# Kernel optimization log

Measured on AMD Instinct MI355X. Metric: run time of the kernel, lower is better.

The kernel has to match this reference:

```python
import jax, jax.numpy as jnp
import numpy as np

N_NODES = 100000
N_EDGES = 3200000
D_NODE = 5            # per-node feature dim
D_IN = 2 * D_NODE     # 10, MLP input dim
D_HID = D_IN * 5      # 50, HIDDEN_DIM_MULTIPLIER = 5


def setup_inputs() -> dict:
    key = jax.random.key(0)
    ks = jax.random.split(key, 8)
    x = jax.random.normal(ks[0], (N_NODES, D_NODE), dtype=jnp.float32)
    edge_index = jax.random.randint(ks[1], (2, N_EDGES), 0, N_NODES, dtype=jnp.int64)
    s1 = 1.0 / np.sqrt(D_IN)
    s2 = 1.0 / np.sqrt(D_HID)
    W1 = jax.random.uniform(ks[2], (D_IN, D_HID), jnp.float32, -s1, s1)
    b1 = jax.random.uniform(ks[3], (D_HID,), jnp.float32, -s1, s1)
    W2 = jax.random.uniform(ks[4], (D_HID, D_HID), jnp.float32, -s2, s2)
    b2 = jax.random.uniform(ks[5], (D_HID,), jnp.float32, -s2, s2)
    W3 = jax.random.uniform(ks[6], (D_HID, 1), jnp.float32, -s2, s2)
    b3 = jax.random.uniform(ks[7], (1,), jnp.float32, -s2, s2)
    return {"x": x, "edge_index": edge_index, "W1": W1, "b1": b1,
            "W2": W2, "b2": b2, "W3": W3, "b3": b3}


def reference(x, edge_index, W1, b1, W2, b2, W3, b3):
    # gather src/tgt node features and concat -> [E, 2*D_NODE]
    ef = jnp.concatenate([x[edge_index[0]], x[edge_index[1]]], axis=-1)
    h = jax.nn.relu(ef @ W1 + b1)
    h = jax.nn.relu(h @ W2 + b2)
    return jax.nn.sigmoid(h @ W3 + b3)  # [E, 1]
```

## Files before the change

kernel.cpp:

```cpp
#include <hip/hip_runtime.h>
#include <hip/hip_bf16.h>

typedef short bf16x8 __attribute__((ext_vector_type(8)));
typedef float f32x4  __attribute__((ext_vector_type(4)));

__device__ inline ushort f2bf(float f) {
    union { float f; uint u; } v; v.f = f;
    uint r = (v.u + 0x7FFFu + ((v.u >> 16) & 1u)) >> 16;
    return (ushort)r;
}
__device__ inline uint packbf(float a, float b) {
    float2 t; t.x = a; t.y = b;
    __hip_bfloat162 h = __float22bfloat162_rn(t);
    union { __hip_bfloat162 h; uint u; } cv; cv.h = h; return cv.u;
}

__global__ __launch_bounds__(256) void pack_x_kernel(
    const float* __restrict__ x, uint4* __restrict__ xp, int N)
{
    int i = blockIdx.x * blockDim.x + threadIdx.x;
    if (i > N) return;
    uint4 o = {0u, 0u, 0u, 0u};
    if (i < N) {
        const float* r = x + (size_t)i * 5;
        o.x = packbf(r[0], r[1]);
        o.y = packbf(r[2], r[3]);
        o.z = packbf(r[4], 1.0f);
    }
    xp[i] = o;
}

__global__ __launch_bounds__(64) void pack_w_kernel(
    const float* __restrict__ W1, const float* __restrict__ b1,
    const float* __restrict__ W2, const float* __restrict__ b2,
    const float* __restrict__ W3, uint4* __restrict__ tab)
{
    const int lane = threadIdx.x;
    const int c = lane & 15;
    const int g = lane >> 4;

    union { ushort s[8]; uint4 q; } u;
    #pragma unroll
    for (int mt = 0; mt < 4; ++mt) {
        #pragma unroll
        for (int d = 0; d < 8; ++d) {
            int k = 8 * g + d;
            int j = 16 * mt + c;
            float v = 0.f;
            if (j < 50) {
                if (k < 5)                 v = W1[k * 50 + j];
                else if (k == 5)           v = b1[j];
                else if (k >= 8 && k < 13) v = W1[(k - 3) * 50 + j];
            } else if (j == 50 && k == 5)  v = 1.0f;
            u.s[d] = f2bf(v);
        }
        tab[mt * 64 + lane] = u.q;
    }
    #pragma unroll
    for (int t = 0; t < 2; ++t) {
        #pragma unroll
        for (int mt = 0; mt < 4; ++mt) {
            #pragma unroll
            for (int d = 0; d < 8; ++d) {
                int hid1 = 16 * (2 * t + (d >> 2)) + 4 * g + (d & 3);
                int j    = 16 * mt + c;
                float v = 0.f;
                if (j < 50) {
                    if (hid1 < 50)       v = W2[hid1 * 50 + j];
                    else if (hid1 == 50) v = b2[j];
                }
                u.s[d] = f2bf(v);
            }
            tab[(4 + t * 4 + mt) * 64 + lane] = u.q;
        }
    }
    union { float f[4]; uint4 q; } wq;
    #pragma unroll
    for (int mt = 0; mt < 4; ++mt) {
        #pragma unroll
        for (int r = 0; r < 4; ++r) {
            int h = 16 * mt + 4 * g + r;
            wq.f[r] = (h < 50) ? W3[h] : 0.f;
        }
        tab[(12 + mt) * 64 + lane] = wq.q;
    }
}

__global__ __launch_bounds__(256, 4) void edge_mlp_mfma4(
    const uint4* __restrict__ xp,
    const uint4* __restrict__ wtab,
    const int* __restrict__ ei,
    const float* __restrict__ b3,
    float* __restrict__ out, int E, int N, int num_tiles)
{
    __shared__ uint4 lds_frag[1024];

    const int tid = threadIdx.x;
    #pragma unroll
    for (int i = 0; i < 4; ++i) lds_frag[tid + 256 * i] = wtab[tid + 256 * i];
    __syncthreads();

    const int w    = tid >> 6;
    const int lane = tid & 63;
    const int c    = lane & 15;
    const int g    = lane >> 4;

    bf16x8 w1f[4];
    #pragma unroll
    for (int mt = 0; mt < 4; ++mt)
        w1f[mt] = *(const bf16x8*)&lds_frag[mt * 64 + lane];
    bf16x8 w2f[2][4];
    #pragma unroll
    for (int t = 0; t < 2; ++t)
        #pragma unroll
        for (int mt = 0; mt < 4; ++mt)
            w2f[t][mt] = *(const bf16x8*)&lds_frag[(4 + t * 4 + mt) * 64 + lane];
    f32x4 w3c[4];
    #pragma unroll
    for (int mt = 0; mt < 4; ++mt)
        w3c[mt] = *(const f32x4*)&lds_frag[(12 + mt) * 64 + lane];
    const float b3s = b3[0];

    for (int bt = blockIdx.x; bt < num_tiles; bt += gridDim.x) {
        const int e0 = bt * 128 + w * 32;

        bf16x8 aEF[2];
        #pragma unroll
        for (int ms = 0; ms < 2; ++ms) {
            int e   = e0 + ms * 16 + c;
            int idx = N;
            if (g < 2) {
                int ee = (e < E) ? e : 0;
                idx = ei[(size_t)g * (size_t)E + (size_t)ee];
            }
            union { uint4 q; bf16x8 v; } u;
            u.q = xp[idx];
            aEF[ms] = u.v;
        }

        #pragma unroll
        for (int ms = 0; ms < 2; ++ms) {
            f32x4 hT[4];
            #pragma unroll
            for (int mt = 0; mt < 4; ++mt) {
                f32x4 z = {0.f, 0.f, 0.f, 0.f};
                hT[mt] = __builtin_amdgcn_mfma_f32_16x16x32_bf16(w1f[mt], aEF[ms], z, 0, 0, 0);
            }
            uint pk[4][2];
            #pragma unroll
            for (int mt = 0; mt < 4; ++mt) {
                float v0 = fmaxf(hT[mt][0], 0.f);
                float v1 = fmaxf(hT[mt][1], 0.f);
                float v2 = fmaxf(hT[mt][2], 0.f);
                float v3 = fmaxf(hT[mt][3], 0.f);
                pk[mt][0] = packbf(v0, v1);
                pk[mt][1] = packbf(v2, v3);
            }
            union { uint u[4]; bf16x8 v; } uu;
            uu.u[0] = pk[0][0]; uu.u[1] = pk[0][1];
            uu.u[2] = pk[1][0]; uu.u[3] = pk[1][1];
            bf16x8 bB0 = uu.v;
            uu.u[0] = pk[2][0]; uu.u[1] = pk[2][1];
            uu.u[2] = pk[3][0]; uu.u[3] = pk[3][1];
            bf16x8 bB1 = uu.v;

            f32x4 h2T[4];
            #pragma unroll
            for (int mt = 0; mt < 4; ++mt) {
                f32x4 z = {0.f, 0.f, 0.f, 0.f};
                h2T[mt] = __builtin_amdgcn_mfma_f32_16x16x32_bf16(w2f[0][mt], bB0, z, 0, 0, 0);
                h2T[mt] = __builtin_amdgcn_mfma_f32_16x16x32_bf16(w2f[1][mt], bB1, h2T[mt], 0, 0, 0);
            }

            float p = 0.f;
            #pragma unroll
            for (int mt = 0; mt < 4; ++mt) {
                #pragma unroll
                for (int r = 0; r < 4; ++r) {
                    float t = fmaxf(h2T[mt][r], 0.f);
                    p = fmaf(t, w3c[mt][r], p);
                }
            }
            p += __shfl_xor(p, 16);
            p += __shfl_xor(p, 32);

            if (g == 0) {
                int e = e0 + ms * 16 + c;
                if (e < E) {
                    float zz = p + b3s;
                    out[e] = 1.f / (1.f + __expf(-zz));
                }
            }
        }
    }
}

extern "C" void kernel_launch(void* const* d_in, const int* in_sizes, int n_in,
                              void* d_out, int out_size, void* d_ws, size_t ws_size,
                              hipStream_t stream) {
    const float* x  = (const float*)d_in[0];
    const int*   ei = (const int*)d_in[1];
    const float* W1 = (const float*)d_in[2];
    const float* b1 = (const float*)d_in[3];
    const float* W2 = (const float*)d_in[4];
    const float* b2 = (const float*)d_in[5];
    const float* W3 = (const float*)d_in[6];
    const float* b3 = (const float*)d_in[7];
    float* out = (float*)d_out;

    int E = in_sizes[1] / 2;
    int N = in_sizes[0] / 5;

    uint4* wtab = (uint4*)d_ws;
    uint4* xp   = (uint4*)((char*)d_ws + 16384);

    pack_w_kernel<<<1, 64, 0, stream>>>(W1, b1, W2, b2, W3, wtab);
    pack_x_kernel<<<(N + 1 + 255) / 256, 256, 0, stream>>>(x, xp, N);

    int num_tiles = (E + 127) / 128;
    int grid = num_tiles < 2048 ? num_tiles : 2048;
    edge_mlp_mfma4<<<grid, 256, 0, stream>>>(xp, wtab, ei, b3, out, E, N, num_tiles);
}
```

Before: 79.97 us.

## Prefetch next edge tile's features and compute final layer with MFMA

The edge MLP kernel now processes 256-edge tiles, with 64 edges per wave. While the current tile is being computed, it issues the index and feature gathers for the next tile, so gather latency overlaps with MFMA work. The third layer (50->1 dot product plus cross-lane shuffle reduction) is replaced by two bf16 MFMAs against a W3 fragment padded into column 0. This removes the shuffles and FMAs but quantizes layer-2 activations and W3 to bf16, and the prefetch buffers raise register pressure.

```diff
diff --git a/kernel.cpp b/kernel.cpp
--- a/kernel.cpp
+++ b/kernel.cpp
@@ -74,30 +74,29 @@
             tab[(4 + t * 4 + mt) * 64 + lane] = u.q;
         }
     }
-    union { float f[4]; uint4 q; } wq;
-    #pragma unroll
-    for (int mt = 0; mt < 4; ++mt) {
-        #pragma unroll
-        for (int r = 0; r < 4; ++r) {
-            int h = 16 * mt + 4 * g + r;
-            wq.f[r] = (h < 50) ? W3[h] : 0.f;
-        }
-        tab[(12 + mt) * 64 + lane] = wq.q;
-    }
-}
-
-__global__ __launch_bounds__(256, 4) void edge_mlp_mfma4(
+    #pragma unroll
+    for (int t = 0; t < 2; ++t) {
+        #pragma unroll
+        for (int d = 0; d < 8; ++d) {
+            int hid = 16 * (2 * t + (d >> 2)) + 4 * g + (d & 3);
+            float v = (c == 0 && hid < 50) ? W3[hid] : 0.f;
+            u.s[d] = f2bf(v);
+        }
+        tab[(12 + t) * 64 + lane] = u.q;
+    }
+}
+
+__global__ __launch_bounds__(256, 4) void edge_mlp_mfma5(
     const uint4* __restrict__ xp,
     const uint4* __restrict__ wtab,
     const int* __restrict__ ei,
     const float* __restrict__ b3,
     float* __restrict__ out, int E, int N, int num_tiles)
 {
-    __shared__ uint4 lds_frag[1024];
+    __shared__ uint4 lds_frag[896];
 
     const int tid = threadIdx.x;
-    #pragma unroll
-    for (int i = 0; i < 4; ++i) lds_frag[tid + 256 * i] = wtab[tid + 256 * i];
+    for (int i = tid; i < 896; i += 256) lds_frag[i] = wtab[i];
     __syncthreads();
 
     const int w    = tid >> 6;
@@ -115,36 +114,51 @@
         #pragma unroll
         for (int mt = 0; mt < 4; ++mt)
             w2f[t][mt] = *(const bf16x8*)&lds_frag[(4 + t * 4 + mt) * 64 + lane];
-    f32x4 w3c[4];
-    #pragma unroll
-    for (int mt = 0; mt < 4; ++mt)
-        w3c[mt] = *(const f32x4*)&lds_frag[(12 + mt) * 64 + lane];
+    bf16x8 w3f[2];
+    #pragma unroll
+    for (int t = 0; t < 2; ++t)
+        w3f[t] = *(const bf16x8*)&lds_frag[(12 + t) * 64 + lane];
     const float b3s = b3[0];
 
-    for (int bt = blockIdx.x; bt < num_tiles; bt += gridDim.x) {
-        const int e0 = bt * 128 + w * 32;
-
-        bf16x8 aEF[2];
-        #pragma unroll
-        for (int ms = 0; ms < 2; ++ms) {
-            int e   = e0 + ms * 16 + c;
-            int idx = N;
+    auto LOADF = [&](int bt_, bf16x8* a) {
+        const int e0 = bt_ * 256 + w * 64;
+        #pragma unroll
+        for (int ms = 0; ms < 4; ++ms) {
+            bf16x8 v = {0, 0, 0, 0, 0, 0, 0, 0};
             if (g < 2) {
+                int e  = e0 + ms * 16 + c;
                 int ee = (e < E) ? e : 0;
-                idx = ei[(size_t)g * (size_t)E + (size_t)ee];
-            }
-            union { uint4 q; bf16x8 v; } u;
-            u.q = xp[idx];
-            aEF[ms] = u.v;
-        }
-
-        #pragma unroll
-        for (int ms = 0; ms < 2; ++ms) {
+                int idx = ei[(size_t)g * (size_t)E + (size_t)ee];
+                union { uint4 q; bf16x8 b; } u;
+                u.q = xp[idx];
+                v = u.b;
+            }
+            a[ms] = v;
+        }
+    };
+
+    int bt = blockIdx.x;
+    if (bt >= num_tiles) return;
+
+    bf16x8 aN[4];
+    LOADF(bt, aN);
+
+    for (; bt < num_tiles; bt += gridDim.x) {
+        bf16x8 aC[4];
+        #pragma unroll
+        for (int i = 0; i < 4; ++i) aC[i] = aN[i];
+        const int btn = bt + gridDim.x;
+        if (btn < num_tiles) LOADF(btn, aN);
+
+        const int e0 = bt * 256 + w * 64;
+
+        #pragma unroll
+        for (int ms = 0; ms < 4; ++ms) {
             f32x4 hT[4];
             #pragma unroll
             for (int mt = 0; mt < 4; ++mt) {
                 f32x4 z = {0.f, 0.f, 0.f, 0.f};
-                hT[mt] = __builtin_amdgcn_mfma_f32_16x16x32_bf16(w1f[mt], aEF[ms], z, 0, 0, 0);
+                hT[mt] = __builtin_amdgcn_mfma_f32_16x16x32_bf16(w1f[mt], aC[ms], z, 0, 0, 0);
             }
             uint pk[4][2];
             #pragma unroll
@@ -171,23 +185,30 @@
                 h2T[mt] = __builtin_amdgcn_mfma_f32_16x16x32_bf16(w2f[0][mt], bB0, z, 0, 0, 0);
                 h2T[mt] = __builtin_amdgcn_mfma_f32_16x16x32_bf16(w2f[1][mt], bB1, h2T[mt], 0, 0, 0);
             }
-
-            float p = 0.f;
-            #pragma unroll
-            for (int mt = 0; mt < 4; ++mt) {
-                #pragma unroll
-                for (int r = 0; r < 4; ++r) {
-                    float t = fmaxf(h2T[mt][r], 0.f);
-                    p = fmaf(t, w3c[mt][r], p);
-                }
-            }
-            p += __shfl_xor(p, 16);
-            p += __shfl_xor(p, 32);
+            #pragma unroll
+            for (int mt = 0; mt < 4; ++mt) {
+                float v0 = fmaxf(h2T[mt][0], 0.f);
+                float v1 = fmaxf(h2T[mt][1], 0.f);
+                float v2 = fmaxf(h2T[mt][2], 0.f);
+                float v3 = fmaxf(h2T[mt][3], 0.f);
+                pk[mt][0] = packbf(v0, v1);
+                pk[mt][1] = packbf(v2, v3);
+            }
+            uu.u[0] = pk[0][0]; uu.u[1] = pk[0][1];
+            uu.u[2] = pk[1][0]; uu.u[3] = pk[1][1];
+            bf16x8 cB0 = uu.v;
+            uu.u[0] = pk[2][0]; uu.u[1] = pk[2][1];
+            uu.u[2] = pk[3][0]; uu.u[3] = pk[3][1];
+            bf16x8 cB1 = uu.v;
+
+            f32x4 z3 = {0.f, 0.f, 0.f, 0.f};
+            f32x4 o3 = __builtin_amdgcn_mfma_f32_16x16x32_bf16(w3f[0], cB0, z3, 0, 0, 0);
+            o3 = __builtin_amdgcn_mfma_f32_16x16x32_bf16(w3f[1], cB1, o3, 0, 0, 0);
 
             if (g == 0) {
                 int e = e0 + ms * 16 + c;
                 if (e < E) {
-                    float zz = p + b3s;
+                    float zz = o3[0] + b3s;
                     out[e] = 1.f / (1.f + __expf(-zz));
                 }
             }
@@ -217,7 +238,7 @@
     pack_w_kernel<<<1, 64, 0, stream>>>(W1, b1, W2, b2, W3, wtab);
     pack_x_kernel<<<(N + 1 + 255) / 256, 256, 0, stream>>>(x, xp, N);
 
-    int num_tiles = (E + 127) / 128;
+    int num_tiles = (E + 255) / 256;
     int grid = num_tiles < 2048 ? num_tiles : 2048;
-    edge_mlp_mfma4<<<grid, 256, 0, stream>>>(xp, wtab, ei, b3, out, E, N, num_tiles);
-}
+    edge_mlp_mfma5<<<grid, 256, 0, stream>>>(xp, wtab, ei, b3, out, E, N, num_tiles);
+}
```

After: 90.03 us. 1.13x slower.
